# Kernel tuning notes

Hardware: AMD Instinct MI355X
Metric: run time of the kernel (lower is better)

Reference implementation:

```python
import jax, jax.numpy as jnp
import numpy as np
from jax.scipy.special import erf

# ---- physical constants (scipy.constants values; FIELD_CONSTANT in eV*Angstrom per e^2) ----
E_CHARGE = 1.602176634e-19
EPS0 = 8.8541878128e-12
PI = float(np.pi)
FIELD_CONSTANT = E_CHARGE * 1e10 / EPS0          # e/(eps0) with Angstrom length units
K_COUL = FIELD_CONSTANT / (4.0 * PI)             # ~14.3996 eV*A

# ---- module hyperparameters (from init_kwargs) ----
SIGMA_D = 0.5
SIGMAS = np.array([0.4, 0.8, 1.2, 1.6], dtype=np.float32)
NUM_RADIAL = 4
OFFSET = 0.1
N_PER_GRAPH = 128
NUM_GRAPHS = 32
M_NODES = N_PER_GRAPH * NUM_GRAPHS

# total_width_factors = sqrt((sigma_d^2 + sigma_r^2)/2)
W_FACTORS = np.sqrt((SIGMA_D**2 + SIGMAS**2) / 2.0).astype(np.float32)      # [R]
# multipole-normalized GTO: C_l = 1/(2^{l+1/2} sigma^{2l+3} Gamma(l+3/2)) => C1/C0 = 1/(3 sigma^2)
L0_FACTORS = np.ones(NUM_RADIAL, dtype=np.float32)                          # ratio = 1 under 'multipoles'
L1_FACTORS = (np.sqrt(3.0) * SIGMAS**2 * (1.0 / (3.0 * SIGMAS**2)) / OFFSET).astype(np.float32)

# 7 duplicate offsets: center, +x, +y, +z, -x, -y, -z
_h = OFFSET
OFFSETS7 = np.array([[0,0,0],[_h,0,0],[0,_h,0],[0,0,_h],[-_h,0,0],[0,-_h,0],[0,0,-_h]], dtype=np.float32)


def _duplicate_charges(sf):
    # sf: [M,4] -> [M,7] FD charge assignment (matches torch slot layout)
    t = 2.0 * OFFSET
    s0, s1, s2, s3 = sf[:, 0], sf[:, 1], sf[:, 2], sf[:, 3]
    return jnp.stack([s0, s3 / t, s1 / t, s2 / t, -s3 / t, -s1 / t, -s2 / t], axis=1)


def _project(sf7):
    # sf7: [M,7,R] per-duplicate scalar features -> [M, 4R]
    M = sf7.shape[0]
    l0 = jnp.asarray(L0_FACTORS) * sf7[:, 0]                                 # [M,R]
    half = 0.5 * jnp.asarray(L1_FACTORS)
    vy = half * (sf7[:, 2] - sf7[:, 5])   # column offset 0 in each triplet
    vz = half * (sf7[:, 3] - sf7[:, 6])   # column offset 1
    vx = half * (sf7[:, 1] - sf7[:, 4])   # column offset 2
    l1 = jnp.stack([vy, vz, vx], axis=-1).reshape(M, 3 * NUM_RADIAL)         # interleaved per radial
    return jnp.concatenate([l0, l1], axis=1)                                 # [M,4R]


def setup_inputs() -> dict:
    key = jax.random.key(0)
    k1, k2 = jax.random.split(key)
    source_feats = jax.random.normal(k1, (M_NODES, 1, 4), dtype=jnp.float32)
    node_positions = 4.0 * jax.random.normal(k2, (M_NODES, 3), dtype=jnp.float32)  # ~Angstrom scale
    batch = jnp.repeat(jnp.arange(NUM_GRAPHS, dtype=jnp.int64), N_PER_GRAPH)
    return {"source_feats": source_feats, "node_positions": node_positions, "batch": batch}


def reference(source_feats, node_positions, batch):
    # density_max_l=1, projection_max_l=1 -> call_density_1_feats_1 path.
    # Assumes equal-size graphs: batch = repeat(arange(G), n) (enforced by setup_inputs).
    sf = source_feats[:, 0, :]                                               # squeeze(-2): [M,4]
    M = sf.shape[0]
    G, n, D, R = NUM_GRAPHS, N_PER_GRAPH, 7 * N_PER_GRAPH, NUM_RADIAL
    w = jnp.asarray(W_FACTORS)                                               # [R]

    charges = _duplicate_charges(sf)                                         # [M,7]
    pos7 = node_positions[:, None, :] + jnp.asarray(OFFSETS7)[None]          # [M,7,3]

    pg = pos7.reshape(G, D, 3)
    cg = charges.reshape(G, D)

    diff = pg[:, :, None, :] - pg[:, None, :, :]                             # [G,D,D,3]
    d2 = jnp.sum(diff * diff, axis=-1)                                       # [G,D,D]
    orig = jnp.arange(D) // 7
    mask = (orig[:, None] != orig[None, :])                                  # exclude same-original-node pairs
    d = jnp.sqrt(jnp.where(mask, d2, 1.0))                                   # safe sqrt (masked entries dummy)
    smooth = erf(0.5 * d[..., None] / w) / (d[..., None] + 1e-6)             # [G,D,D,R]
    smooth = smooth * mask[None, :, :, None]
    # scatter_sum over senders i into receivers j
    sfeat = K_COUL * jnp.einsum('gi,gijr->gjr', cg, smooth)                  # [G,D,R]
    sfeat = sfeat.reshape(M, 7, R)

    # GTOSelfInteractionBlock (reconstructed): interactions among a node's own
    # 7 duplicates with analytic d->0 limit erf(x)/x -> 1/(w*sqrt(pi)).
    off = jnp.asarray(OFFSETS7)
    ds = jnp.linalg.norm(off[:, None, :] - off[None, :, :], axis=-1)          # [7,7]
    phi = jnp.where(ds[..., None] > 0.0,
                    erf(0.5 * ds[..., None] / w) / (ds[..., None] + 1e-6),
                    1.0 / (w * np.sqrt(PI)))                                  # [7,7,R]
    sself = K_COUL * jnp.einsum('mi,ijr->mjr', charges, phi)                  # [M,7,R]

    features = _project(sfeat)
    self_terms = _project(sself)
    features = features + self_terms                                          # include_self_interaction=True
    return features, self_terms
```

## Files before the change

kernel.cpp:

```cpp
#include <hip/hip_runtime.h>
#include <math.h>

namespace {

constexpr int   MTOT = 4096;
constexpr float H    = 0.1f;

constexpr float W0 = 0.45276925690687087f;
constexpr float W1 = 0.66708320320631664f;
constexpr float W2 = 0.91923881554251174f;
constexpr float W3 = 1.18532695911296985f;

constexpr float KCOUL   = 14.399645478425669f;
constexpr float HALF_L1 = 2.8867513459481287f;
constexpr float SQRTPI  = 1.7724538509055159f;

constexpr float K0 = 1.1043153f, K1 = 0.74953184f, K2 = 0.54392830f, K3 = 0.42182454f;

constexpr float PK0 = 0.5195472f, PK1 = 0.3526314f, PK2 = 0.2559019f, PK3 = 0.1984558f;
constexpr float C20 = -1.7593842f, C21 = -0.8105028f, C22 = -0.4268329f, C23 = -0.2567073f;
constexpr float EA1 = 0.3480242f, EA2 = -0.0958798f, EA3 = 0.7478556f;
constexpr float RCP_H = 9.9999000f, RCP_HS2 = 7.0710178f, RCP_2H = 4.9999750f;

constexpr int   TABN  = 512;
constexpr float TAB_H = 0.015f;
constexpr float INV_H = 66.666664f;

__device__ __forceinline__ float fast_rcp(float x)  { return __builtin_amdgcn_rcpf(x); }
__device__ __forceinline__ float fast_rsq(float x)  { return __builtin_amdgcn_rsqf(x); }
__device__ __forceinline__ float fast_exp2(float x) { return __builtin_amdgcn_exp2f(x); }

__device__ __forceinline__ float erf_q(float d, float d2, float pk, float c2) {
  float t = fast_rcp(__builtin_fmaf(d, pk, 1.0f));
  float poly = t * __builtin_fmaf(t, __builtin_fmaf(t, EA3, EA2), EA1);
  return poly * fast_exp2(d2 * c2);
}

__device__ __forceinline__ float project_one(const float* S, int k) {
  if (k < 4) return S[k];
  int q = k - 4;
  int r = q / 3;
  int comp = q - 3 * r;
  int j1, j2;
  if (comp == 0)      { j1 = 2; j2 = 5; }
  else if (comp == 1) { j1 = 3; j2 = 6; }
  else                { j1 = 1; j2 = 4; }
  return HALF_L1 * (S[j1 * 4 + r] - S[j2 * 4 + r]);
}

__global__ __launch_bounds__(896, 4) void es_main(
    const float* __restrict__ sf,
    const float* __restrict__ pos,
    float* __restrict__ out)
{
  __shared__ float4 s_pos4[128];
  __shared__ float4 s_chg4[128];
  __shared__ float2 s_tab[4][TABN];
  __shared__ float  s_tmp[4][TABN + 1];
  __shared__ float4 s_part[8 * 112];
  __shared__ float  s_feat[448];
  __shared__ float  s_self[448];

  const int b   = blockIdx.x;
  const int g   = b >> 3;
  const int nb  = b & 7;
  const int tid = threadIdx.x;

  if (tid < 128) {
    const float* p = pos + (size_t)(g * 128 + tid) * 3;
    s_pos4[tid] = make_float4(p[0], p[1], p[2], 0.0f);
  } else if (tid < 256) {
    const int i = tid - 128;
    const float4 s = ((const float4*)sf)[g * 128 + i];
    s_chg4[i] = make_float4(s.x, 5.0f * s.w, 5.0f * s.y, 5.0f * s.z);
  }
  if (tid <= TABN) {
    const float d = tid * TAB_H;
    s_tmp[0][tid] = erff(K0 * d);
    s_tmp[1][tid] = erff(K1 * d);
    s_tmp[2][tid] = erff(K2 * d);
    s_tmp[3][tid] = erff(K3 * d);
  }
  __syncthreads();
  if (tid < TABN) {
#pragma unroll
    for (int r = 0; r < 4; ++r) {
      const float v = s_tmp[r][tid];
      s_tab[r][tid] = make_float2(v, s_tmp[r][tid + 1] - v);
    }
  }
  __syncthreads();

  const int site_local = tid % 112;
  const int chunk      = tid / 112;
  const int sl   = nb * 112 + site_local;
  const int jown = (sl * 9363) >> 16;
  const int aoff = sl - jown * 7;

  const float4 cp = s_pos4[jown];
  const float tx = cp.x + ((aoff == 1) ? H : (aoff == 4) ? -H : 0.0f);
  const float ty = cp.y + ((aoff == 2) ? H : (aoff == 5) ? -H : 0.0f);
  const float tz = cp.z + ((aoff == 3) ? H : (aoff == 6) ? -H : 0.0f);

  float a0 = 0.f, a1 = 0.f, a2 = 0.f, a3 = 0.f;

  auto acc = [&](float d2raw, float c) {
    float d2 = fmaxf(d2raw, 1e-12f);
    float rd = fast_rsq(d2);
    float cv = c * rd;
    float t  = (d2 * rd) * INV_H;
    int  idx = (int)t;
    float f  = t - (float)idx;
    idx = (idx < TABN - 1) ? idx : (TABN - 1);
    const float2 e0 = s_tab[0][idx];
    const float2 e1 = s_tab[1][idx];
    const float2 e2 = s_tab[2][idx];
    const float2 e3 = s_tab[3][idx];
    a0 = __builtin_fmaf(cv, __builtin_fmaf(e0.y, f, e0.x), a0);
    a1 = __builtin_fmaf(cv, __builtin_fmaf(e1.y, f, e1.x), a1);
    a2 = __builtin_fmaf(cv, __builtin_fmaf(e2.y, f, e2.x), a2);
    a3 = __builtin_fmaf(cv, __builtin_fmaf(e3.y, f, e3.x), a3);
  };

  const int j0 = chunk * 16;
#pragma unroll 2
  for (int jj = 0; jj < 16; ++jj) {
    const int j = j0 + jj;
    const float4 p4 = s_pos4[j];
    const float4 c4 = s_chg4[j];
    const float vx = tx - p4.x;
    const float vy = ty - p4.y;
    const float vz = tz - p4.z;
    const float v2 = __builtin_fmaf(vx, vx, __builtin_fmaf(vy, vy, vz * vz));
    const float w2 = v2 + 0.01f;
    const bool own = (j == jown);
    acc(v2,                            (own & (aoff == 0)) ? 0.0f :  c4.x);
    acc(__builtin_fmaf(vx, -0.2f, w2), (own & (aoff == 1)) ? 0.0f :  c4.y);
    acc(__builtin_fmaf(vy, -0.2f, w2), (own & (aoff == 2)) ? 0.0f :  c4.z);
    acc(__builtin_fmaf(vz, -0.2f, w2), (own & (aoff == 3)) ? 0.0f :  c4.w);
    acc(__builtin_fmaf(vx,  0.2f, w2), (own & (aoff == 4)) ? 0.0f : -c4.y);
    acc(__builtin_fmaf(vy,  0.2f, w2), (own & (aoff == 5)) ? 0.0f : -c4.z);
    acc(__builtin_fmaf(vz,  0.2f, w2), (own & (aoff == 6)) ? 0.0f : -c4.w);
  }

  s_part[chunk * 112 + site_local] = make_float4(a0, a1, a2, a3);
  __syncthreads();

  if (tid < 448) {
    const int site = tid >> 2;
    const int r    = tid & 3;
    const float* pf = (const float*)s_part;
    float tot = 0.f;
#pragma unroll
    for (int c = 0; c < 8; ++c) tot += pf[c * 448 + tid];

    const float w  = (r == 0) ? W0  : (r == 1) ? W1  : (r == 2) ? W2  : W3;
    const float pk = (r == 0) ? PK0 : (r == 1) ? PK1 : (r == 2) ? PK2 : PK3;
    const float c2 = (r == 0) ? C20 : (r == 1) ? C21 : (r == 2) ? C22 : C23;
    const float diag = fast_rcp(w * SQRTPI);
    const float ph1 = (1.f - erf_q(0.1f,        0.01f, pk, c2)) * RCP_H;
    const float ph2 = (1.f - erf_q(0.14142136f, 0.02f, pk, c2)) * RCP_HS2;
    const float ph3 = (1.f - erf_q(0.2f,        0.04f, pk, c2)) * RCP_2H;

    const int jn = (site * 9363) >> 16;
    const int ba = site - jn * 7;
    const float4 c4 = s_chg4[nb * 16 + jn];
    float selfSum = 0.f, ca = 0.f;
#pragma unroll
    for (int i = 0; i < 7; ++i) {
      const float ci = (i == 0) ?  c4.x : (i == 1) ?  c4.y : (i == 2) ?  c4.z :
                       (i == 3) ?  c4.w : (i == 4) ? -c4.y : (i == 5) ? -c4.z : -c4.w;
      float ph;
      if (i == ba)                             ph = diag;
      else if (i == 0 || ba == 0)              ph = ph1;
      else if ((i - ba == 3) || (ba - i == 3)) ph = ph3;
      else                                     ph = ph2;
      selfSum = __builtin_fmaf(ci, ph, selfSum);
      if (i == ba) ca = ci;
    }
    s_self[tid] = KCOUL * selfSum;
    s_feat[tid] = KCOUL * __builtin_fmaf(ca, diag, tot);
  }
  __syncthreads();

  if (tid < 256) {
    const int node = tid >> 4;
    const int k    = tid & 15;
    const int m    = g * 128 + nb * 16 + node;
    float vf = project_one(&s_feat[node * 28], k);
    float vs = project_one(&s_self[node * 28], k);
    out[m * 16 + k]             = vf;
    out[MTOT * 16 + m * 16 + k] = vs;
  }
}

}

extern "C" void kernel_launch(void* const* d_in, const int* in_sizes, int n_in,
                              void* d_out, int out_size, void* d_ws, size_t ws_size,
                              hipStream_t stream) {
  const float* sf  = (const float*)d_in[0];
  const float* pos = (const float*)d_in[1];
  float* out = (float*)d_out;
  es_main<<<256, 896, 0, stream>>>(sf, pos, out);
}
```

Measured before the change: 82.17 us.

## Morton-sort nodes and skip erf lookup for far pairs with saturated erf

Nodes in each graph are sorted by a Morton key of coarse spatial cells so that neighbouring sites land in the same wave. When every lane of a wave has a sender beyond a cutoff distance (erf saturated), the table lookup is replaced by a plain 1/d accumulation shared across all four radial channels. The erf table is also repacked into float4 value and delta arrays so each lookup takes two loads instead of four. The intent is to remove interpolation and LDS traffic for distant pairs. This costs a 128-way rank sort, an indirection when writing outputs, and a small accuracy approximation for far pairs.

```diff
diff --git a/kernel.cpp b/kernel.cpp
--- a/kernel.cpp
+++ b/kernel.cpp
@@ -25,6 +25,8 @@
 constexpr int   TABN  = 512;
 constexpr float TAB_H = 0.015f;
 constexpr float INV_H = 66.666664f;
+
+constexpr float SAT2 = 49.4f;
 
 __device__ __forceinline__ float fast_rcp(float x)  { return __builtin_amdgcn_rcpf(x); }
 __device__ __forceinline__ float fast_rsq(float x)  { return __builtin_amdgcn_rsqf(x); }
@@ -48,31 +50,43 @@
   return HALF_L1 * (S[j1 * 4 + r] - S[j2 * 4 + r]);
 }
 
+__device__ __forceinline__ unsigned spread3(int v) {
+  return (unsigned)((v & 1) | ((v & 2) << 2) | ((v & 4) << 4));
+}
+
 __global__ __launch_bounds__(896, 4) void es_main(
     const float* __restrict__ sf,
     const float* __restrict__ pos,
     float* __restrict__ out)
 {
-  __shared__ float4 s_pos4[128];
-  __shared__ float4 s_chg4[128];
-  __shared__ float2 s_tab[4][TABN];
-  __shared__ float  s_tmp[4][TABN + 1];
-  __shared__ float4 s_part[8 * 112];
-  __shared__ float  s_feat[448];
-  __shared__ float  s_self[448];
+  __shared__ float4   s_pos4[128];
+  __shared__ float4   s_chg4[128];
+  __shared__ int      s_orig[128];
+  __shared__ unsigned s_key[128];
+  __shared__ float4   s_tabV[TABN];
+  __shared__ float4   s_tabD[TABN];
+  __shared__ float    s_tmp[4][TABN + 1];
+  __shared__ float4   s_part[8 * 112];
+  __shared__ float    s_feat[448];
+  __shared__ float    s_self[448];
 
   const int b   = blockIdx.x;
   const int g   = b >> 3;
   const int nb  = b & 7;
   const int tid = threadIdx.x;
 
+  float px = 0.f, py = 0.f, pz = 0.f;
+  float4 myc = make_float4(0.f, 0.f, 0.f, 0.f);
   if (tid < 128) {
     const float* p = pos + (size_t)(g * 128 + tid) * 3;
-    s_pos4[tid] = make_float4(p[0], p[1], p[2], 0.0f);
-  } else if (tid < 256) {
-    const int i = tid - 128;
-    const float4 s = ((const float4*)sf)[g * 128 + i];
-    s_chg4[i] = make_float4(s.x, 5.0f * s.w, 5.0f * s.y, 5.0f * s.z);
+    px = p[0]; py = p[1]; pz = p[2];
+    const float4 s = ((const float4*)sf)[g * 128 + tid];
+    myc = make_float4(s.x, 5.0f * s.w, 5.0f * s.y, 5.0f * s.z);
+    int cx = (int)((px + 16.0f) * 0.25f); cx = (cx < 0) ? 0 : (cx > 7 ? 7 : cx);
+    int cy = (int)((py + 16.0f) * 0.25f); cy = (cy < 0) ? 0 : (cy > 7 ? 7 : cy);
+    int cz = (int)((pz + 16.0f) * 0.25f); cz = (cz < 0) ? 0 : (cz > 7 ? 7 : cz);
+    unsigned mort = spread3(cx) | (spread3(cy) << 1) | (spread3(cz) << 2);
+    s_key[tid] = (mort << 7) | (unsigned)tid;
   }
   if (tid <= TABN) {
     const float d = tid * TAB_H;
@@ -82,12 +96,21 @@
     s_tmp[3][tid] = erff(K3 * d);
   }
   __syncthreads();
+
+  if (tid < 128) {
+    const unsigned mykey = s_key[tid];
+    int rank = 0;
+    for (int t = 0; t < 128; ++t) rank += (s_key[t] < mykey) ? 1 : 0;
+    s_pos4[rank] = make_float4(px, py, pz, 0.0f);
+    s_chg4[rank] = myc;
+    s_orig[rank] = tid;
+  }
   if (tid < TABN) {
-#pragma unroll
-    for (int r = 0; r < 4; ++r) {
-      const float v = s_tmp[r][tid];
-      s_tab[r][tid] = make_float2(v, s_tmp[r][tid + 1] - v);
-    }
+    const float v0 = s_tmp[0][tid], v1 = s_tmp[1][tid];
+    const float v2v = s_tmp[2][tid], v3 = s_tmp[3][tid];
+    s_tabV[tid] = make_float4(v0, v1, v2v, v3);
+    s_tabD[tid] = make_float4(s_tmp[0][tid + 1] - v0, s_tmp[1][tid + 1] - v1,
+                              s_tmp[2][tid + 1] - v2v, s_tmp[3][tid + 1] - v3);
   }
   __syncthreads();
 
@@ -102,9 +125,9 @@
   const float ty = cp.y + ((aoff == 2) ? H : (aoff == 5) ? -H : 0.0f);
   const float tz = cp.z + ((aoff == 3) ? H : (aoff == 6) ? -H : 0.0f);
 
-  float a0 = 0.f, a1 = 0.f, a2 = 0.f, a3 = 0.f;
-
-  auto acc = [&](float d2raw, float c) {
+  float a0 = 0.f, a1 = 0.f, a2 = 0.f, a3 = 0.f, Ssat = 0.f;
+
+  auto acc_full = [&](float d2raw, float c) {
     float d2 = fmaxf(d2raw, 1e-12f);
     float rd = fast_rsq(d2);
     float cv = c * rd;
@@ -112,18 +135,16 @@
     int  idx = (int)t;
     float f  = t - (float)idx;
     idx = (idx < TABN - 1) ? idx : (TABN - 1);
-    const float2 e0 = s_tab[0][idx];
-    const float2 e1 = s_tab[1][idx];
-    const float2 e2 = s_tab[2][idx];
-    const float2 e3 = s_tab[3][idx];
-    a0 = __builtin_fmaf(cv, __builtin_fmaf(e0.y, f, e0.x), a0);
-    a1 = __builtin_fmaf(cv, __builtin_fmaf(e1.y, f, e1.x), a1);
-    a2 = __builtin_fmaf(cv, __builtin_fmaf(e2.y, f, e2.x), a2);
-    a3 = __builtin_fmaf(cv, __builtin_fmaf(e3.y, f, e3.x), a3);
+    f = fminf(f, 1.0f);
+    const float4 V = s_tabV[idx];
+    const float4 D = s_tabD[idx];
+    a0 = __builtin_fmaf(cv, __builtin_fmaf(D.x, f, V.x), a0);
+    a1 = __builtin_fmaf(cv, __builtin_fmaf(D.y, f, V.y), a1);
+    a2 = __builtin_fmaf(cv, __builtin_fmaf(D.z, f, V.z), a2);
+    a3 = __builtin_fmaf(cv, __builtin_fmaf(D.w, f, V.w), a3);
   };
 
   const int j0 = chunk * 16;
-#pragma unroll 2
   for (int jj = 0; jj < 16; ++jj) {
     const int j = j0 + jj;
     const float4 p4 = s_pos4[j];
@@ -132,16 +153,28 @@
     const float vy = ty - p4.y;
     const float vz = tz - p4.z;
     const float v2 = __builtin_fmaf(vx, vx, __builtin_fmaf(vy, vy, vz * vz));
-    const float w2 = v2 + 0.01f;
-    const bool own = (j == jown);
-    acc(v2,                            (own & (aoff == 0)) ? 0.0f :  c4.x);
-    acc(__builtin_fmaf(vx, -0.2f, w2), (own & (aoff == 1)) ? 0.0f :  c4.y);
-    acc(__builtin_fmaf(vy, -0.2f, w2), (own & (aoff == 2)) ? 0.0f :  c4.z);
-    acc(__builtin_fmaf(vz, -0.2f, w2), (own & (aoff == 3)) ? 0.0f :  c4.w);
-    acc(__builtin_fmaf(vx,  0.2f, w2), (own & (aoff == 4)) ? 0.0f : -c4.y);
-    acc(__builtin_fmaf(vy,  0.2f, w2), (own & (aoff == 5)) ? 0.0f : -c4.z);
-    acc(__builtin_fmaf(vz,  0.2f, w2), (own & (aoff == 6)) ? 0.0f : -c4.w);
-  }
+    if (__any(v2 < SAT2)) {
+      const float w2 = v2 + 0.01f;
+      const bool own = (j == jown);
+      acc_full(v2,                            (own & (aoff == 0)) ? 0.0f :  c4.x);
+      acc_full(__builtin_fmaf(vx, -0.2f, w2), (own & (aoff == 1)) ? 0.0f :  c4.y);
+      acc_full(__builtin_fmaf(vy, -0.2f, w2), (own & (aoff == 2)) ? 0.0f :  c4.z);
+      acc_full(__builtin_fmaf(vz, -0.2f, w2), (own & (aoff == 3)) ? 0.0f :  c4.w);
+      acc_full(__builtin_fmaf(vx,  0.2f, w2), (own & (aoff == 4)) ? 0.0f : -c4.y);
+      acc_full(__builtin_fmaf(vy,  0.2f, w2), (own & (aoff == 5)) ? 0.0f : -c4.z);
+      acc_full(__builtin_fmaf(vz,  0.2f, w2), (own & (aoff == 6)) ? 0.0f : -c4.w);
+    } else {
+      const float w2 = v2 + 0.01f;
+      Ssat += c4.x * fast_rsq(v2);
+      Ssat = __builtin_fmaf( c4.y, fast_rsq(__builtin_fmaf(vx, -0.2f, w2)), Ssat);
+      Ssat = __builtin_fmaf( c4.z, fast_rsq(__builtin_fmaf(vy, -0.2f, w2)), Ssat);
+      Ssat = __builtin_fmaf( c4.w, fast_rsq(__builtin_fmaf(vz, -0.2f, w2)), Ssat);
+      Ssat = __builtin_fmaf(-c4.y, fast_rsq(__builtin_fmaf(vx,  0.2f, w2)), Ssat);
+      Ssat = __builtin_fmaf(-c4.z, fast_rsq(__builtin_fmaf(vy,  0.2f, w2)), Ssat);
+      Ssat = __builtin_fmaf(-c4.w, fast_rsq(__builtin_fmaf(vz,  0.2f, w2)), Ssat);
+    }
+  }
+  a0 += Ssat; a1 += Ssat; a2 += Ssat; a3 += Ssat;
 
   s_part[chunk * 112 + site_local] = make_float4(a0, a1, a2, a3);
   __syncthreads();
@@ -186,7 +219,7 @@
   if (tid < 256) {
     const int node = tid >> 4;
     const int k    = tid & 15;
-    const int m    = g * 128 + nb * 16 + node;
+    const int m    = g * 128 + s_orig[nb * 16 + node];
     float vf = project_one(&s_feat[node * 28], k);
     float vs = project_one(&s_self[node * 28], k);
     out[m * 16 + k]             = vf;
```

Result: faster. 75.21 us (-8.5%).
